# Kernel tuning notes

Measured on AMD Instinct MI355X. Metric: run time of the kernel, lower is better.

Reference implementation:

```python
import jax, jax.numpy as jnp
import numpy as np

HIDDEN = 1024
FFN = 2048
NUM_EXPERTS = 8
TOP_K = 2
BATCH, SEQ = 2, 1024


def setup_inputs() -> dict:
    key = jax.random.key(0)
    k0, k1, k2, k3, k4 = jax.random.split(key, 5)
    scale = 0.02
    hidden_states = jax.random.normal(k0, (BATCH, SEQ, HIDDEN), dtype=jnp.float32)
    gate_w = jax.random.normal(k1, (NUM_EXPERTS, HIDDEN), dtype=jnp.float32) * scale
    w1 = jax.random.normal(k2, (NUM_EXPERTS, FFN, HIDDEN), dtype=jnp.float32) * scale  # gate proj
    w3 = jax.random.normal(k3, (NUM_EXPERTS, FFN, HIDDEN), dtype=jnp.float32) * scale  # up proj
    w2 = jax.random.normal(k4, (NUM_EXPERTS, HIDDEN, FFN), dtype=jnp.float32) * scale  # down proj
    return {"hidden_states": hidden_states, "gate_w": gate_w, "w1": w1, "w2": w2, "w3": w3}


def reference(hidden_states, gate_w, w1, w2, w3):
    B, S, D = hidden_states.shape
    x = hidden_states.reshape(-1, D)                         # [T, D]
    T = x.shape[0]
    # Router: logits -> fp32 softmax -> top-k -> renormalize
    router_logits = jnp.einsum("td,ed->te", x, gate_w)       # [T, E]
    routing_weights = jax.nn.softmax(router_logits.astype(jnp.float32), axis=1)
    top_vals, top_idx = jax.lax.top_k(routing_weights, TOP_K)  # [T, K]
    top_vals = top_vals / jnp.sum(top_vals, axis=-1, keepdims=True)
    top_vals = top_vals.astype(x.dtype)
    # Per-token-per-expert combine weight (0 for unselected experts)
    w_te = jnp.zeros((T, NUM_EXPERTS), dtype=x.dtype)
    w_te = w_te.at[jnp.arange(T)[:, None], top_idx].add(top_vals)  # [T, E]
    # Fused experts: silu(x W1^T) * (x W3^T) -> W2^T, weighted combine
    g = jax.nn.silu(jnp.einsum("td,efd->tef", x, w1))        # [T, E, F]
    u = jnp.einsum("td,efd->tef", x, w3)                     # [T, E, F]
    y = jnp.einsum("tef,edf->ted", g * u, w2)                # [T, E, D]
    out = jnp.einsum("ted,te->td", y, w_te)                  # [T, D]
    return out.reshape(B, S, D), router_logits
```

## Files before the change

### kernel.cpp

```cpp
#include <hip/hip_runtime.h>
#include <hip/hip_bf16.h>
#include <stdint.h>

#define HIDDEN  1024
#define FFN_DIM 2048
#define NEXP    8
#define NTOK    2048
#define MAXROWS 5120

typedef short bf16x8 __attribute__((ext_vector_type(8)));
typedef float f32x4  __attribute__((ext_vector_type(4)));

static const size_t OFF_CNT  = 0;
static const size_t OFF_BASE = 64;
static const size_t OFF_TOK  = 128;
static const size_t OFF_WGT  = OFF_TOK + (size_t)NEXP*NTOK*4;
static const size_t OFF_XBF  = 131328;
static const size_t XBF_B    = (size_t)NTOK*HIDDEN*2;
static const size_t OFF_H    = OFF_XBF + XBF_B;
static const size_t H_B      = (size_t)MAXROWS*FFN_DIM*2;
static const size_t WS_NEED  = OFF_H + H_B;

__device__ __forceinline__ unsigned short f2bf(float f) {
  union { float f; unsigned u; } a; a.f = f;
  unsigned r = a.u + 0x7fff + ((a.u >> 16) & 1);
  return (unsigned short)(r >> 16);
}

__device__ __forceinline__ uint4 cvt8(float4 a, float4 b) {
  uint4 r;
  asm("v_cvt_pk_bf16_f32 %0, %1, %2" : "=v"(r.x) : "v"(a.x), "v"(a.y));
  asm("v_cvt_pk_bf16_f32 %0, %1, %2" : "=v"(r.y) : "v"(a.z), "v"(a.w));
  asm("v_cvt_pk_bf16_f32 %0, %1, %2" : "=v"(r.z) : "v"(b.x), "v"(b.y));
  asm("v_cvt_pk_bf16_f32 %0, %1, %2" : "=v"(r.w) : "v"(b.z), "v"(b.w));
  return r;
}

__device__ __forceinline__ void ld_g2l16(const void* gsrc, void* ldst) {
  __builtin_amdgcn_global_load_lds(
      (const __attribute__((address_space(1))) unsigned int*)gsrc,
      (__attribute__((address_space(3))) unsigned int*)ldst, 16, 0, 0);
}

__global__ __launch_bounds__(256) void router_kernel(
    const float* __restrict__ x, const float* __restrict__ gw,
    float* __restrict__ logits, int* __restrict__ cnt,
    int* __restrict__ tok, float* __restrict__ wgt)
{
  const int t   = blockIdx.x;
  const int tid = threadIdx.x;
  float4 xv = ((const float4*)(x + (size_t)t * HIDDEN))[tid];
  float p[NEXP];
#pragma unroll
  for (int e = 0; e < NEXP; ++e) {
    float4 gv = ((const float4*)(gw + (size_t)e * HIDDEN))[tid];
    p[e] = xv.x * gv.x + xv.y * gv.y + xv.z * gv.z + xv.w * gv.w;
  }
#pragma unroll
  for (int e = 0; e < NEXP; ++e) {
#pragma unroll
    for (int off = 32; off > 0; off >>= 1)
      p[e] += __shfl_down(p[e], off, 64);
  }
  __shared__ float red[4][NEXP];
  const int wv = tid >> 6, ln = tid & 63;
  if (ln == 0) {
#pragma unroll
    for (int e = 0; e < NEXP; ++e) red[wv][e] = p[e];
  }
  __syncthreads();
  if (tid == 0) {
    float l[NEXP];
#pragma unroll
    for (int e = 0; e < NEXP; ++e) {
      l[e] = red[0][e] + red[1][e] + red[2][e] + red[3][e];
      logits[(size_t)t * NEXP + e] = l[e];
    }
    int i0 = 0;
#pragma unroll
    for (int e = 1; e < NEXP; ++e) if (l[e] > l[i0]) i0 = e;
    int i1 = (i0 == 0) ? 1 : 0;
#pragma unroll
    for (int e = 0; e < NEXP; ++e) if (e != i0 && l[e] > l[i1]) i1 = e;
    float w0 = 1.f / (1.f + expf(l[i1] - l[i0]));
    float w1 = 1.f - w0;
    int s0 = atomicAdd(&cnt[i0], 1);
    tok[i0 * NTOK + s0] = t;  wgt[i0 * NTOK + s0] = w0;
    int s1 = atomicAdd(&cnt[i1], 1);
    tok[i1 * NTOK + s1] = t;  wgt[i1 * NTOK + s1] = w1;
  }
}

__global__ void prefix_kernel(const int* __restrict__ cnt, int* __restrict__ base) {
  if (threadIdx.x == 0 && blockIdx.x == 0) {
    int b = 0;
#pragma unroll
    for (int e = 0; e < NEXP; ++e) { base[e] = b; b += ((cnt[e] + 127) >> 7) << 7; }
    base[NEXP] = b;
  }
}

__global__ __launch_bounds__(256) void cvt_kernel(
    const float* __restrict__ src, unsigned short* __restrict__ dst, int n4)
{
  int i = blockIdx.x * blockDim.x + threadIdx.x;
  const int stride = gridDim.x * blockDim.x;
  for (; i < n4; i += stride) {
    float4 v = ((const float4*)src)[i];
    ushort4 o;
    o.x = f2bf(v.x); o.y = f2bf(v.y); o.z = f2bf(v.z); o.w = f2bf(v.w);
    ((ushort4*)dst)[i] = o;
  }
}

__global__ __launch_bounds__(512, 4) void gemm1_kernel(
    const unsigned short* __restrict__ xbf,
    const float* __restrict__ w1f,
    const float* __restrict__ w3f,
    const int* __restrict__ cnt, const int* __restrict__ base,
    const int* __restrict__ tok,
    unsigned short* __restrict__ H)
{
  const int bid  = blockIdx.x;
  const int e    = bid & 7;
  const int slot = bid >> 3;
  const int mt   = slot & 15;
  const int nt   = slot >> 4;
  const int n = cnt[e];
  if (mt * 128 >= n) return;
  const int t = threadIdx.x;
  const int w = t >> 6, l = t & 63;

  __shared__ unsigned short Xs [128 * 64];
  __shared__ unsigned short W1s[128 * 64];
  __shared__ unsigned short W3s[128 * 64];
  __shared__ int stok[128];

  if (t < 128) {
    int idx = mt * 128 + t;
    stok[t] = tok[e * NTOK + min(idx, n - 1)];
  }
  __syncthreads();

  const int r0 = t >> 3;
  const size_t tok0 = (size_t)stok[r0];
  const size_t tok1 = (size_t)stok[64 + r0];
  const int kp = (((t & 7) ^ ((t >> 3) & 7)) << 3);

  const float* w1e = w1f + (size_t)e * FFN_DIM * HIDDEN + (size_t)(nt * 128) * HIDDEN;
  const float* w3e = w3f + (size_t)e * FFN_DIM * HIDDEN + (size_t)(nt * 128) * HIDDEN;
  const float* w1p0 = w1e + (size_t)r0        * HIDDEN + kp;
  const float* w1p1 = w1e + (size_t)(64 + r0) * HIDDEN + kp;
  const float* w3p0 = w3e + (size_t)r0        * HIDDEN + kp;
  const float* w3p1 = w3e + (size_t)(64 + r0) * HIDDEN + kp;

  uint4* lw1a = (uint4*)((char*)W1s + t * 16);
  uint4* lw1b = (uint4*)((char*)W1s + 8192 + t * 16);
  uint4* lw3a = (uint4*)((char*)W3s + t * 16);
  uint4* lw3b = (uint4*)((char*)W3s + 8192 + t * 16);
  char* ldsX = (char*)Xs + w * 1024;

  f32x4 acc1[4][2], acc3[4][2];
#pragma unroll
  for (int i = 0; i < 4; ++i)
#pragma unroll
    for (int j = 0; j < 2; ++j) { acc1[i][j] = (f32x4)0.f; acc3[i][j] = (f32x4)0.f; }

  const int Moff = (w & 1) * 64;
  const int Noff = (w >> 1) * 32;
  const int lr = l & 15;
  const int lg = l >> 4;

  for (int kb = 0; kb < HIDDEN / 64; ++kb) {
    __syncthreads();
    const int kofs = kb * 64 + kp;
    ld_g2l16(xbf + tok0 * HIDDEN + kofs, ldsX);
    ld_g2l16(xbf + tok1 * HIDDEN + kofs, ldsX + 8192);
    {
      const int ko = kb * 64;
      float4 a0 = *(const float4*)(w1p0 + ko);
      float4 a1 = *(const float4*)(w1p0 + ko + 4);
      float4 a2 = *(const float4*)(w1p1 + ko);
      float4 a3 = *(const float4*)(w1p1 + ko + 4);
      float4 b0 = *(const float4*)(w3p0 + ko);
      float4 b1 = *(const float4*)(w3p0 + ko + 4);
      float4 b2 = *(const float4*)(w3p1 + ko);
      float4 b3 = *(const float4*)(w3p1 + ko + 4);
      *lw1a = cvt8(a0, a1);
      *lw1b = cvt8(a2, a3);
      *lw3a = cvt8(b0, b1);
      *lw3b = cvt8(b2, b3);
    }
    __syncthreads();
#pragma unroll
    for (int s = 0; s < 2; ++s) {
      const int ug = 4 * s + lg;
      bf16x8 a[4], b1v[2], b3v[2];
#pragma unroll
      for (int mi = 0; mi < 4; ++mi) {
        const int R = Moff + mi * 16 + lr;
        a[mi] = *(const bf16x8*)&Xs[R * 64 + ((ug ^ (lr & 7)) << 3)];
      }
#pragma unroll
      for (int ni = 0; ni < 2; ++ni) {
        const int R = Noff + ni * 16 + lr;
        b1v[ni] = *(const bf16x8*)&W1s[R * 64 + ((ug ^ (lr & 7)) << 3)];
        b3v[ni] = *(const bf16x8*)&W3s[R * 64 + ((ug ^ (lr & 7)) << 3)];
      }
#pragma unroll
      for (int mi = 0; mi < 4; ++mi)
#pragma unroll
        for (int ni = 0; ni < 2; ++ni) {
          acc1[mi][ni] = __builtin_amdgcn_mfma_f32_16x16x32_bf16(a[mi], b1v[ni], acc1[mi][ni], 0, 0, 0);
          acc3[mi][ni] = __builtin_amdgcn_mfma_f32_16x16x32_bf16(a[mi], b3v[ni], acc3[mi][ni], 0, 0, 0);
        }
    }
  }

  const size_t rbase = (size_t)base[e] + (size_t)mt * 128;
#pragma unroll
  for (int mi = 0; mi < 4; ++mi)
#pragma unroll
    for (int ni = 0; ni < 2; ++ni)
#pragma unroll
      for (int j = 0; j < 4; ++j) {
        int row = Moff + mi * 16 + lg * 4 + j;
        int col = nt * 128 + Noff + ni * 16 + lr;
        float s1 = acc1[mi][ni][j], s3 = acc3[mi][ni][j];
        float h = (s1 / (1.f + __expf(-s1))) * s3;
        H[(rbase + row) * FFN_DIM + col] = f2bf(h);
      }
}

__global__ __launch_bounds__(512, 4) void gemm2_kernel(
    const unsigned short* __restrict__ H,
    const float* __restrict__ w2f,
    const int* __restrict__ cnt, const int* __restrict__ base,
    const int* __restrict__ tok, const float* __restrict__ wgt,
    float* __restrict__ out)
{
  const int bid  = blockIdx.x;
  const int e    = bid & 7;
  const int slot = bid >> 3;
  const int mt   = slot & 15;
  const int nt   = slot >> 4;
  const int n = cnt[e];
  if (mt * 128 >= n) return;
  const int t = threadIdx.x;
  const int w = t >> 6, l = t & 63;

  __shared__ unsigned short Hs[128 * 64];
  __shared__ unsigned short Ws[128 * 64];
  __shared__ int   stok[128];
  __shared__ float swgt[128];

  if (t < 128) {
    int idx = mt * 128 + t;
    int ok = idx < n;
    stok[t] = ok ? tok[e * NTOK + idx] : -1;
    swgt[t] = ok ? wgt[e * NTOK + idx] : 0.f;
  }

  const int r0 = t >> 3;
  const int kp = (((t & 7) ^ ((t >> 3) & 7)) << 3);
  const unsigned short* He = H + (size_t)(base[e] + mt * 128) * FFN_DIM;
  const float* w2e  = w2f + (size_t)e * HIDDEN * FFN_DIM + (size_t)(nt * 128) * FFN_DIM;
  const float* w2p0 = w2e + (size_t)r0        * FFN_DIM + kp;
  const float* w2p1 = w2e + (size_t)(64 + r0) * FFN_DIM + kp;

  uint4* lwa = (uint4*)((char*)Ws + t * 16);
  uint4* lwb = (uint4*)((char*)Ws + 8192 + t * 16);
  char* ldsH = (char*)Hs + w * 1024;

  f32x4 acc[4][2];
#pragma unroll
  for (int i = 0; i < 4; ++i)
#pragma unroll
    for (int j = 0; j < 2; ++j) acc[i][j] = (f32x4)0.f;

  const int Moff = (w & 1) * 64;
  const int Noff = (w >> 1) * 32;
  const int lr = l & 15;
  const int lg = l >> 4;

  for (int kb = 0; kb < FFN_DIM / 64; ++kb) {
    __syncthreads();
    const int kofs = kb * 64 + kp;
    ld_g2l16(He + (size_t)r0 * FFN_DIM + kofs,        ldsH);
    ld_g2l16(He + (size_t)(64 + r0) * FFN_DIM + kofs, ldsH + 8192);
    {
      const int ko = kb * 64;
      float4 a0 = *(const float4*)(w2p0 + ko);
      float4 a1 = *(const float4*)(w2p0 + ko + 4);
      float4 a2 = *(const float4*)(w2p1 + ko);
      float4 a3 = *(const float4*)(w2p1 + ko + 4);
      *lwa = cvt8(a0, a1);
      *lwb = cvt8(a2, a3);
    }
    __syncthreads();
#pragma unroll
    for (int s = 0; s < 2; ++s) {
      const int ug = 4 * s + lg;
      bf16x8 a[4], b[2];
#pragma unroll
      for (int mi = 0; mi < 4; ++mi) {
        const int R = Moff + mi * 16 + lr;
        a[mi] = *(const bf16x8*)&Hs[R * 64 + ((ug ^ (lr & 7)) << 3)];
      }
#pragma unroll
      for (int ni = 0; ni < 2; ++ni) {
        const int R = Noff + ni * 16 + lr;
        b[ni] = *(const bf16x8*)&Ws[R * 64 + ((ug ^ (lr & 7)) << 3)];
      }
#pragma unroll
      for (int mi = 0; mi < 4; ++mi)
#pragma unroll
        for (int ni = 0; ni < 2; ++ni)
          acc[mi][ni] = __builtin_amdgcn_mfma_f32_16x16x32_bf16(a[mi], b[ni], acc[mi][ni], 0, 0, 0);
    }
  }

#pragma unroll
  for (int mi = 0; mi < 4; ++mi)
#pragma unroll
    for (int ni = 0; ni < 2; ++ni)
#pragma unroll
      for (int j = 0; j < 4; ++j) {
        int row = Moff + mi * 16 + lg * 4 + j;
        int tk = stok[row];
        if (tk >= 0) {
          int col = nt * 128 + Noff + ni * 16 + lr;
          atomicAdd(&out[(size_t)tk * HIDDEN + col], swgt[row] * acc[mi][ni][j]);
        }
      }
}

#define TT 12
#define FC 256
#define NCHUNK (FFN_DIM / FC)

__global__ __launch_bounds__(256) void moe_ffn_kernel(
    const float* __restrict__ x,
    const float* __restrict__ w1, const float* __restrict__ w2,
    const float* __restrict__ w3,
    const int* __restrict__ cnt, const int* __restrict__ tok,
    const float* __restrict__ wgt, float* __restrict__ out)
{
  const int e  = blockIdx.y;
  const int n  = cnt[e];
  const int ts = blockIdx.x * TT;
  if (ts >= n) return;
  const int tid = threadIdx.x;

  __shared__ float xs[TT * HIDDEN];
  __shared__ float hc[TT * FC];
  __shared__ int   stok[TT];
  __shared__ float swgt[TT];

  if (tid < TT) {
    int idx = ts + tid;
    int tk  = (idx < n) ? tok[e * NTOK + idx] : -1;
    stok[tid] = tk;
    swgt[tid] = (idx < n) ? wgt[e * NTOK + idx] : 0.f;
  }
  __syncthreads();
#pragma unroll
  for (int i = 0; i < TT; ++i) {
    int tk = stok[i];
    float4 v = make_float4(0.f, 0.f, 0.f, 0.f);
    if (tk >= 0) v = ((const float4*)(x + (size_t)tk * HIDDEN))[tid];
    ((float4*)(xs + i * HIDDEN))[tid] = v;
  }
  __syncthreads();

  const float* w1e = w1 + (size_t)e * FFN_DIM * HIDDEN;
  const float* w3e = w3 + (size_t)e * FFN_DIM * HIDDEN;
  const float* w2e = w2 + (size_t)e * HIDDEN * FFN_DIM;

  float yacc[4][TT];
#pragma unroll
  for (int j = 0; j < 4; ++j)
#pragma unroll
    for (int t = 0; t < TT; ++t) yacc[j][t] = 0.f;

  for (int c = 0; c < NCHUNK; ++c) {
    const int f = c * FC + tid;
    const float4* r1 = (const float4*)(w1e + (size_t)f * HIDDEN);
    const float4* r3 = (const float4*)(w3e + (size_t)f * HIDDEN);
    float a1[TT], a3[TT];
#pragma unroll
    for (int t = 0; t < TT; ++t) { a1[t] = 0.f; a3[t] = 0.f; }
    for (int k = 0; k < HIDDEN / 4; ++k) {
      float4 v1 = r1[k];
      float4 v3 = r3[k];
#pragma unroll
      for (int t = 0; t < TT; ++t) {
        float4 xv = *(const float4*)(xs + t * HIDDEN + 4 * k);
        a1[t] += xv.x * v1.x + xv.y * v1.y + xv.z * v1.z + xv.w * v1.w;
        a3[t] += xv.x * v3.x + xv.y * v3.y + xv.z * v3.z + xv.w * v3.w;
      }
    }
    __syncthreads();
#pragma unroll
    for (int t = 0; t < TT; ++t) {
      float g  = a1[t];
      float sg = g / (1.f + __expf(-g));
      hc[t * FC + tid] = sg * a3[t];
    }
    __syncthreads();
    const float4* r20 = (const float4*)(w2e + (size_t)(tid      ) * FFN_DIM + c * FC);
    const float4* r21 = (const float4*)(w2e + (size_t)(tid + 256) * FFN_DIM + c * FC);
    const float4* r22 = (const float4*)(w2e + (size_t)(tid + 512) * FFN_DIM + c * FC);
    const float4* r23 = (const float4*)(w2e + (size_t)(tid + 768) * FFN_DIM + c * FC);
    for (int k = 0; k < FC / 4; ++k) {
      float4 wv0 = r20[k], wv1 = r21[k], wv2 = r22[k], wv3 = r23[k];
#pragma unroll
      for (int t = 0; t < TT; ++t) {
        float4 hv = *(const float4*)(hc + t * FC + 4 * k);
        yacc[0][t] += hv.x * wv0.x + hv.y * wv0.y + hv.z * wv0.z + hv.w * wv0.w;
        yacc[1][t] += hv.x * wv1.x + hv.y * wv1.y + hv.z * wv1.z + hv.w * wv1.w;
        yacc[2][t] += hv.x * wv2.x + hv.y * wv2.y + hv.z * wv2.z + hv.w * wv2.w;
        yacc[3][t] += hv.x * wv3.x + hv.y * wv3.y + hv.z * wv3.z + hv.w * wv3.w;
      }
    }
  }

#pragma unroll
  for (int t = 0; t < TT; ++t) {
    int tk = stok[t];
    if (tk < 0) continue;
    float wt = swgt[t];
    float* orow = out + (size_t)tk * HIDDEN;
    atomicAdd(orow + tid,       wt * yacc[0][t]);
    atomicAdd(orow + tid + 256, wt * yacc[1][t]);
    atomicAdd(orow + tid + 512, wt * yacc[2][t]);
    atomicAdd(orow + tid + 768, wt * yacc[3][t]);
  }
}

extern "C" void kernel_launch(void* const* d_in, const int* in_sizes, int n_in,
                              void* d_out, int out_size, void* d_ws, size_t ws_size,
                              hipStream_t stream) {
  const float* x  = (const float*)d_in[0];
  const float* gw = (const float*)d_in[1];
  const float* w1 = (const float*)d_in[2];
  const float* w2 = (const float*)d_in[3];
  const float* w3 = (const float*)d_in[4];
  float* out    = (float*)d_out;
  float* logits = out + (size_t)NTOK * HIDDEN;

  char* ws = (char*)d_ws;
  int*   cnt  = (int*)(ws + OFF_CNT);
  int*   base = (int*)(ws + OFF_BASE);
  int*   tokp = (int*)(ws + OFF_TOK);
  float* wgtp = (float*)(ws + OFF_WGT);

  hipMemsetAsync(out, 0, (size_t)NTOK * HIDDEN * sizeof(float), stream);
  hipMemsetAsync(cnt, 0, NEXP * sizeof(int), stream);

  router_kernel<<<NTOK, 256, 0, stream>>>(x, gw, logits, cnt, tokp, wgtp);

  if (ws_size >= WS_NEED) {
    unsigned short* xbf  = (unsigned short*)(ws + OFF_XBF);
    unsigned short* Hbuf = (unsigned short*)(ws + OFF_H);

    cvt_kernel<<<512, 256, 0, stream>>>(x, xbf, (int)(NTOK * HIDDEN / 4));
    prefix_kernel<<<1, 64, 0, stream>>>(cnt, base);

    gemm1_kernel<<<NEXP * 16 * 16, 512, 0, stream>>>(xbf, w1, w3, cnt, base, tokp, Hbuf);
    gemm2_kernel<<<NEXP * 16 * 8, 512, 0, stream>>>(Hbuf, w2, cnt, base, tokp, wgtp, out);
  } else {
    dim3 grid((NTOK + TT - 1) / TT, NEXP);
    moe_ffn_kernel<<<grid, 256, 0, stream>>>(x, w1, w2, w3, cnt, tokp, wgtp, out);
  }
}
```

Before: 227.1 us.

## Stream fp32 weights to LDS asynchronously, shrink GEMM tiles, split-K down-projection, fuse x conversion

Fp32 weights now go straight into LDS through async global_load_lds with a swizzled layout, and are converted to bf16 only when fragments are read. This removes the register round trip and the convert before each LDS store. Both GEMMs move to 256-thread blocks with 128x64 tiles, and the down-projection is split across two K halves to raise the block count. The x-to-bf16 conversion is folded into the router kernel, so the separate conversion launch goes away. In exchange, fp32 tiles double the LDS traffic, each fragment read is converted repeatedly across waves, and the split-K doubles the atomic adds to the output.

Result: faster. 196.8 us (-13.3%).

```diff
diff --git a/kernel.cpp b/kernel.cpp
--- a/kernel.cpp
+++ b/kernel.cpp
@@ -27,13 +27,13 @@
   return (unsigned short)(r >> 16);
 }
 
-__device__ __forceinline__ uint4 cvt8(float4 a, float4 b) {
-  uint4 r;
-  asm("v_cvt_pk_bf16_f32 %0, %1, %2" : "=v"(r.x) : "v"(a.x), "v"(a.y));
-  asm("v_cvt_pk_bf16_f32 %0, %1, %2" : "=v"(r.y) : "v"(a.z), "v"(a.w));
-  asm("v_cvt_pk_bf16_f32 %0, %1, %2" : "=v"(r.z) : "v"(b.x), "v"(b.y));
-  asm("v_cvt_pk_bf16_f32 %0, %1, %2" : "=v"(r.w) : "v"(b.z), "v"(b.w));
-  return r;
+__device__ __forceinline__ bf16x8 cvt8b(float4 a, float4 b) {
+  union { uint4 u; bf16x8 v; } r;
+  asm("v_cvt_pk_bf16_f32 %0, %1, %2" : "=v"(r.u.x) : "v"(a.x), "v"(a.y));
+  asm("v_cvt_pk_bf16_f32 %0, %1, %2" : "=v"(r.u.y) : "v"(a.z), "v"(a.w));
+  asm("v_cvt_pk_bf16_f32 %0, %1, %2" : "=v"(r.u.z) : "v"(b.x), "v"(b.y));
+  asm("v_cvt_pk_bf16_f32 %0, %1, %2" : "=v"(r.u.w) : "v"(b.z), "v"(b.w));
+  return r.v;
 }
 
 __device__ __forceinline__ void ld_g2l16(const void* gsrc, void* ldst) {
@@ -45,11 +45,17 @@
 __global__ __launch_bounds__(256) void router_kernel(
     const float* __restrict__ x, const float* __restrict__ gw,
     float* __restrict__ logits, int* __restrict__ cnt,
-    int* __restrict__ tok, float* __restrict__ wgt)
+    int* __restrict__ tok, float* __restrict__ wgt,
+    unsigned short* __restrict__ xbf)
 {
   const int t   = blockIdx.x;
   const int tid = threadIdx.x;
   float4 xv = ((const float4*)(x + (size_t)t * HIDDEN))[tid];
+  if (xbf) {
+    ushort4 o;
+    o.x = f2bf(xv.x); o.y = f2bf(xv.y); o.z = f2bf(xv.z); o.w = f2bf(xv.w);
+    ((ushort4*)(xbf + (size_t)t * HIDDEN))[tid] = o;
+  }
   float p[NEXP];
 #pragma unroll
   for (int e = 0; e < NEXP; ++e) {
@@ -100,20 +106,7 @@
   }
 }
 
-__global__ __launch_bounds__(256) void cvt_kernel(
-    const float* __restrict__ src, unsigned short* __restrict__ dst, int n4)
-{
-  int i = blockIdx.x * blockDim.x + threadIdx.x;
-  const int stride = gridDim.x * blockDim.x;
-  for (; i < n4; i += stride) {
-    float4 v = ((const float4*)src)[i];
-    ushort4 o;
-    o.x = f2bf(v.x); o.y = f2bf(v.y); o.z = f2bf(v.z); o.w = f2bf(v.w);
-    ((ushort4*)dst)[i] = o;
-  }
-}
-
-__global__ __launch_bounds__(512, 4) void gemm1_kernel(
+__global__ __launch_bounds__(256, 3) void gemm1_kernel(
     const unsigned short* __restrict__ xbf,
     const float* __restrict__ w1f,
     const float* __restrict__ w3f,
@@ -131,34 +124,23 @@
   const int t = threadIdx.x;
   const int w = t >> 6, l = t & 63;
 
-  __shared__ unsigned short Xs [128 * 64];
-  __shared__ unsigned short W1s[128 * 64];
-  __shared__ unsigned short W3s[128 * 64];
-  __shared__ int stok[128];
-
-  if (t < 128) {
-    int idx = mt * 128 + t;
-    stok[t] = tok[e * NTOK + min(idx, n - 1)];
-  }
-  __syncthreads();
-
-  const int r0 = t >> 3;
-  const size_t tok0 = (size_t)stok[r0];
-  const size_t tok1 = (size_t)stok[64 + r0];
-  const int kp = (((t & 7) ^ ((t >> 3) & 7)) << 3);
-
-  const float* w1e = w1f + (size_t)e * FFN_DIM * HIDDEN + (size_t)(nt * 128) * HIDDEN;
-  const float* w3e = w3f + (size_t)e * FFN_DIM * HIDDEN + (size_t)(nt * 128) * HIDDEN;
-  const float* w1p0 = w1e + (size_t)r0        * HIDDEN + kp;
-  const float* w1p1 = w1e + (size_t)(64 + r0) * HIDDEN + kp;
-  const float* w3p0 = w3e + (size_t)r0        * HIDDEN + kp;
-  const float* w3p1 = w3e + (size_t)(64 + r0) * HIDDEN + kp;
-
-  uint4* lw1a = (uint4*)((char*)W1s + t * 16);
-  uint4* lw1b = (uint4*)((char*)W1s + 8192 + t * 16);
-  uint4* lw3a = (uint4*)((char*)W3s + t * 16);
-  uint4* lw3b = (uint4*)((char*)W3s + 8192 + t * 16);
-  char* ldsX = (char*)Xs + w * 1024;
+  __shared__ unsigned short Xs[128 * 64];
+  __shared__ float W1s[64 * 64];
+  __shared__ float W3s[64 * 64];
+
+  const int xr   = t >> 3;
+  const int xkey = ((t & 7) ^ (xr & 7)) << 3;
+  const unsigned short* xp[4];
+#pragma unroll
+  for (int c = 0; c < 4; ++c) {
+    int row = min(mt * 128 + c * 32 + xr, n - 1);
+    xp[c] = xbf + (size_t)tok[e * NTOK + row] * HIDDEN + xkey;
+  }
+
+  const int wr   = t >> 4;
+  const int wkey = ((t & 15) ^ wr) << 2;
+  const float* w1p = w1f + (size_t)e * FFN_DIM * HIDDEN + ((size_t)nt * 64 + wr) * HIDDEN + wkey;
+  const float* w3p = w3f + (size_t)e * FFN_DIM * HIDDEN + ((size_t)nt * 64 + wr) * HIDDEN + wkey;
 
   f32x4 acc1[4][2], acc3[4][2];
 #pragma unroll
@@ -173,47 +155,41 @@
 
   for (int kb = 0; kb < HIDDEN / 64; ++kb) {
     __syncthreads();
-    const int kofs = kb * 64 + kp;
-    ld_g2l16(xbf + tok0 * HIDDEN + kofs, ldsX);
-    ld_g2l16(xbf + tok1 * HIDDEN + kofs, ldsX + 8192);
-    {
-      const int ko = kb * 64;
-      float4 a0 = *(const float4*)(w1p0 + ko);
-      float4 a1 = *(const float4*)(w1p0 + ko + 4);
-      float4 a2 = *(const float4*)(w1p1 + ko);
-      float4 a3 = *(const float4*)(w1p1 + ko + 4);
-      float4 b0 = *(const float4*)(w3p0 + ko);
-      float4 b1 = *(const float4*)(w3p0 + ko + 4);
-      float4 b2 = *(const float4*)(w3p1 + ko);
-      float4 b3 = *(const float4*)(w3p1 + ko + 4);
-      *lw1a = cvt8(a0, a1);
-      *lw1b = cvt8(a2, a3);
-      *lw3a = cvt8(b0, b1);
-      *lw3b = cvt8(b2, b3);
+    const int ko = kb * 64;
+#pragma unroll
+    for (int c = 0; c < 4; ++c)
+      ld_g2l16(xp[c] + ko, (char*)Xs + c * 4096 + w * 1024);
+#pragma unroll
+    for (int c = 0; c < 4; ++c) {
+      ld_g2l16(w1p + (size_t)c * 16 * HIDDEN + ko, (char*)W1s + c * 4096 + w * 1024);
+      ld_g2l16(w3p + (size_t)c * 16 * HIDDEN + ko, (char*)W3s + c * 4096 + w * 1024);
     }
     __syncthreads();
 #pragma unroll
     for (int s = 0; s < 2; ++s) {
-      const int ug = 4 * s + lg;
-      bf16x8 a[4], b1v[2], b3v[2];
+      const int ub = 4 * s + lg;
+      bf16x8 a[4];
 #pragma unroll
       for (int mi = 0; mi < 4; ++mi) {
         const int R = Moff + mi * 16 + lr;
-        a[mi] = *(const bf16x8*)&Xs[R * 64 + ((ug ^ (lr & 7)) << 3)];
+        a[mi] = *(const bf16x8*)((const char*)Xs + R * 128 + ((ub ^ (R & 7)) << 4));
       }
 #pragma unroll
       for (int ni = 0; ni < 2; ++ni) {
-        const int R = Noff + ni * 16 + lr;
-        b1v[ni] = *(const bf16x8*)&W1s[R * 64 + ((ug ^ (lr & 7)) << 3)];
-        b3v[ni] = *(const bf16x8*)&W3s[R * 64 + ((ug ^ (lr & 7)) << 3)];
-      }
-#pragma unroll
-      for (int mi = 0; mi < 4; ++mi)
-#pragma unroll
-        for (int ni = 0; ni < 2; ++ni) {
-          acc1[mi][ni] = __builtin_amdgcn_mfma_f32_16x16x32_bf16(a[mi], b1v[ni], acc1[mi][ni], 0, 0, 0);
-          acc3[mi][ni] = __builtin_amdgcn_mfma_f32_16x16x32_bf16(a[mi], b3v[ni], acc3[mi][ni], 0, 0, 0);
+        const int R  = Noff + ni * 16 + lr;
+        const int p0 = (2 * ub) ^ (R & 15);
+        float4 lo1 = *(const float4*)((const char*)W1s + R * 256 + (p0 << 4));
+        float4 hi1 = *(const float4*)((const char*)W1s + R * 256 + ((p0 ^ 1) << 4));
+        float4 lo3 = *(const float4*)((const char*)W3s + R * 256 + (p0 << 4));
+        float4 hi3 = *(const float4*)((const char*)W3s + R * 256 + ((p0 ^ 1) << 4));
+        bf16x8 b1 = cvt8b(lo1, hi1);
+        bf16x8 b3 = cvt8b(lo3, hi3);
+#pragma unroll
+        for (int mi = 0; mi < 4; ++mi) {
+          acc1[mi][ni] = __builtin_amdgcn_mfma_f32_16x16x32_bf16(a[mi], b1, acc1[mi][ni], 0, 0, 0);
+          acc3[mi][ni] = __builtin_amdgcn_mfma_f32_16x16x32_bf16(a[mi], b3, acc3[mi][ni], 0, 0, 0);
         }
+      }
     }
   }
 
@@ -225,14 +201,14 @@
 #pragma unroll
       for (int j = 0; j < 4; ++j) {
         int row = Moff + mi * 16 + lg * 4 + j;
-        int col = nt * 128 + Noff + ni * 16 + lr;
+        int col = nt * 64 + Noff + ni * 16 + lr;
         float s1 = acc1[mi][ni][j], s3 = acc3[mi][ni][j];
         float h = (s1 / (1.f + __expf(-s1))) * s3;
         H[(rbase + row) * FFN_DIM + col] = f2bf(h);
       }
 }
 
-__global__ __launch_bounds__(512, 4) void gemm2_kernel(
+__global__ __launch_bounds__(256, 4) void gemm2_kernel(
     const unsigned short* __restrict__ H,
     const float* __restrict__ w2f,
     const int* __restrict__ cnt, const int* __restrict__ base,
@@ -243,14 +219,15 @@
   const int e    = bid & 7;
   const int slot = bid >> 3;
   const int mt   = slot & 15;
-  const int nt   = slot >> 4;
+  const int nt   = (slot >> 4) & 15;
+  const int sk   = slot >> 8;
   const int n = cnt[e];
   if (mt * 128 >= n) return;
   const int t = threadIdx.x;
   const int w = t >> 6, l = t & 63;
 
   __shared__ unsigned short Hs[128 * 64];
-  __shared__ unsigned short Ws[128 * 64];
+  __shared__ float W2s[64 * 64];
   __shared__ int   stok[128];
   __shared__ float swgt[128];
 
@@ -261,16 +238,14 @@
     swgt[t] = ok ? wgt[e * NTOK + idx] : 0.f;
   }
 
-  const int r0 = t >> 3;
-  const int kp = (((t & 7) ^ ((t >> 3) & 7)) << 3);
-  const unsigned short* He = H + (size_t)(base[e] + mt * 128) * FFN_DIM;
-  const float* w2e  = w2f + (size_t)e * HIDDEN * FFN_DIM + (size_t)(nt * 128) * FFN_DIM;
-  const float* w2p0 = w2e + (size_t)r0        * FFN_DIM + kp;
-  const float* w2p1 = w2e + (size_t)(64 + r0) * FFN_DIM + kp;
-
-  uint4* lwa = (uint4*)((char*)Ws + t * 16);
-  uint4* lwb = (uint4*)((char*)Ws + 8192 + t * 16);
-  char* ldsH = (char*)Hs + w * 1024;
+  const int xr   = t >> 3;
+  const int xkey = ((t & 7) ^ (xr & 7)) << 3;
+  const unsigned short* Hp = H + (size_t)(base[e] + mt * 128 + xr) * FFN_DIM
+                               + sk * (FFN_DIM / 2) + xkey;
+  const int wr   = t >> 4;
+  const int wkey = ((t & 15) ^ wr) << 2;
+  const float* w2p = w2f + (size_t)e * HIDDEN * FFN_DIM + ((size_t)nt * 64 + wr) * FFN_DIM
+                        + sk * (FFN_DIM / 2) + wkey;
 
   f32x4 acc[4][2];
 #pragma unroll
@@ -283,40 +258,36 @@
   const int lr = l & 15;
   const int lg = l >> 4;
 
-  for (int kb = 0; kb < FFN_DIM / 64; ++kb) {
-    __syncthreads();
-    const int kofs = kb * 64 + kp;
-    ld_g2l16(He + (size_t)r0 * FFN_DIM + kofs,        ldsH);
-    ld_g2l16(He + (size_t)(64 + r0) * FFN_DIM + kofs, ldsH + 8192);
-    {
-      const int ko = kb * 64;
-      float4 a0 = *(const float4*)(w2p0 + ko);
-      float4 a1 = *(const float4*)(w2p0 + ko + 4);
-      float4 a2 = *(const float4*)(w2p1 + ko);
-      float4 a3 = *(const float4*)(w2p1 + ko + 4);
-      *lwa = cvt8(a0, a1);
-      *lwb = cvt8(a2, a3);
-    }
+  for (int kb = 0; kb < FFN_DIM / 2 / 64; ++kb) {
+    __syncthreads();
+    const int ko = kb * 64;
+#pragma unroll
+    for (int c = 0; c < 4; ++c)
+      ld_g2l16(Hp + (size_t)c * 32 * FFN_DIM + ko, (char*)Hs + c * 4096 + w * 1024);
+#pragma unroll
+    for (int c = 0; c < 4; ++c)
+      ld_g2l16(w2p + (size_t)c * 16 * FFN_DIM + ko, (char*)W2s + c * 4096 + w * 1024);
     __syncthreads();
 #pragma unroll
     for (int s = 0; s < 2; ++s) {
-      const int ug = 4 * s + lg;
-      bf16x8 a[4], b[2];
+      const int ub = 4 * s + lg;
+      bf16x8 a[4];
 #pragma unroll
       for (int mi = 0; mi < 4; ++mi) {
         const int R = Moff + mi * 16 + lr;
-        a[mi] = *(const bf16x8*)&Hs[R * 64 + ((ug ^ (lr & 7)) << 3)];
+        a[mi] = *(const bf16x8*)((const char*)Hs + R * 128 + ((ub ^ (R & 7)) << 4));
       }
 #pragma unroll
       for (int ni = 0; ni < 2; ++ni) {
-        const int R = Noff + ni * 16 + lr;
-        b[ni] = *(const bf16x8*)&Ws[R * 64 + ((ug ^ (lr & 7)) << 3)];
-      }
-#pragma unroll
-      for (int mi = 0; mi < 4; ++mi)
-#pragma unroll
-        for (int ni = 0; ni < 2; ++ni)
-          acc[mi][ni] = __builtin_amdgcn_mfma_f32_16x16x32_bf16(a[mi], b[ni], acc[mi][ni], 0, 0, 0);
+        const int R  = Noff + ni * 16 + lr;
+        const int p0 = (2 * ub) ^ (R & 15);
+        float4 lo = *(const float4*)((const char*)W2s + R * 256 + (p0 << 4));
+        float4 hi = *(const float4*)((const char*)W2s + R * 256 + ((p0 ^ 1) << 4));
+        bf16x8 b = cvt8b(lo, hi);
+#pragma unroll
+        for (int mi = 0; mi < 4; ++mi)
+          acc[mi][ni] = __builtin_amdgcn_mfma_f32_16x16x32_bf16(a[mi], b, acc[mi][ni], 0, 0, 0);
+      }
     }
   }
 
@@ -329,7 +300,7 @@
         int row = Moff + mi * 16 + lg * 4 + j;
         int tk = stok[row];
         if (tk >= 0) {
-          int col = nt * 128 + Noff + ni * 16 + lr;
+          int col = nt * 64 + Noff + ni * 16 + lr;
           atomicAdd(&out[(size_t)tk * HIDDEN + col], swgt[row] * acc[mi][ni][j]);
         }
       }
@@ -455,20 +426,19 @@
   int*   tokp = (int*)(ws + OFF_TOK);
   float* wgtp = (float*)(ws + OFF_WGT);
 
+  const bool big = (ws_size >= WS_NEED);
+  unsigned short* xbf  = big ? (unsigned short*)(ws + OFF_XBF) : (unsigned short*)0;
+  unsigned short* Hbuf = big ? (unsigned short*)(ws + OFF_H)   : (unsigned short*)0;
+
   hipMemsetAsync(out, 0, (size_t)NTOK * HIDDEN * sizeof(float), stream);
   hipMemsetAsync(cnt, 0, NEXP * sizeof(int), stream);
 
-  router_kernel<<<NTOK, 256, 0, stream>>>(x, gw, logits, cnt, tokp, wgtp);
-
-  if (ws_size >= WS_NEED) {
-    unsigned short* xbf  = (unsigned short*)(ws + OFF_XBF);
-    unsigned short* Hbuf = (unsigned short*)(ws + OFF_H);
-
-    cvt_kernel<<<512, 256, 0, stream>>>(x, xbf, (int)(NTOK * HIDDEN / 4));
+  router_kernel<<<NTOK, 256, 0, stream>>>(x, gw, logits, cnt, tokp, wgtp, xbf);
+
+  if (big) {
     prefix_kernel<<<1, 64, 0, stream>>>(cnt, base);
-
-    gemm1_kernel<<<NEXP * 16 * 16, 512, 0, stream>>>(xbf, w1, w3, cnt, base, tokp, Hbuf);
-    gemm2_kernel<<<NEXP * 16 * 8, 512, 0, stream>>>(Hbuf, w2, cnt, base, tokp, wgtp, out);
+    gemm1_kernel<<<NEXP * 16 * 32, 256, 0, stream>>>(xbf, w1, w3, cnt, base, tokp, Hbuf);
+    gemm2_kernel<<<NEXP * 16 * 16 * 2, 256, 0, stream>>>(Hbuf, w2, cnt, base, tokp, wgtp, out);
   } else {
     dim3 grid((NTOK + TT - 1) / TT, NEXP);
     moe_ffn_kernel<<<grid, 256, 0, stream>>>(x, w1, w2, w3, cnt, tokp, wgtp, out);
```
